# Kernel optimization log

Measured on AMD Instinct MI355X. Metric: run time of the kernel, lower is better.

Reference implementation:

```python
import jax, jax.numpy as jnp
import numpy as np

N = 768       # num nodes
E = 12288     # num edges (avg degree 16)
D_IN = 6
H = 256       # hidden_dim
TEMPERATURE = 1.0


def gcn_conv(x, W, b, src, dst, n):
    """PyG GCNConv: add self-loops, symmetric deg^-1/2 normalization, then xW aggregation + bias."""
    h = x @ W  # [n, H]
    loop = jnp.arange(n, dtype=src.dtype)
    s = jnp.concatenate([src, loop])
    d = jnp.concatenate([dst, loop])
    deg = jax.ops.segment_sum(jnp.ones(s.shape, dtype=h.dtype), d, num_segments=n)
    dinv = jnp.where(deg > 0, jax.lax.rsqrt(deg), 0.0)
    norm = dinv[s] * dinv[d]  # [E+n]
    out = jax.ops.segment_sum(h[s] * norm[:, None], d, num_segments=n)
    return out + b


def setup_inputs() -> dict:
    key = jax.random.key(0)
    ks = jax.random.split(key, 10)
    sc = lambda fan: np.float32(1.0 / np.sqrt(fan))
    x = jax.random.normal(ks[0], (N, D_IN), jnp.float32)
    edge_index = jax.random.randint(ks[1], (2, E), 0, N, dtype=jnp.int32)
    Wc1 = jax.random.normal(ks[2], (D_IN, H), jnp.float32) * sc(D_IN)
    bc1 = jnp.zeros((H,), jnp.float32)
    Wc2 = jax.random.normal(ks[3], (H, H), jnp.float32) * sc(H)
    bc2 = jnp.zeros((H,), jnp.float32)
    We1 = jax.random.normal(ks[4], (2 * H, H), jnp.float32) * sc(2 * H)
    be1 = jax.random.normal(ks[5], (H,), jnp.float32) * sc(2 * H)
    We2 = jax.random.normal(ks[6], (H, 1), jnp.float32) * sc(H)
    be2 = jax.random.normal(ks[7], (1,), jnp.float32) * sc(H)
    return {"x": x, "edge_index": edge_index, "Wc1": Wc1, "bc1": bc1,
            "Wc2": Wc2, "bc2": bc2, "We1": We1, "be1": be1, "We2": We2, "be2": be2}


def reference(x, edge_index, Wc1, bc1, Wc2, bc2, We1, be1, We2, be2):
    src, dst = edge_index[0], edge_index[1]
    h = jax.nn.elu(gcn_conv(x, Wc1, bc1, src, dst, N))
    h = gcn_conv(h, Wc2, bc2, src, dst, N)  # [N, H]
    # edge scorer: Linear(cat([x_i, x_j])) == x_i @ We1[:H] + x_j @ We1[H:] + be1
    ai = h @ We1[:H]   # [N, H], contribution of x_i (row node)
    aj = h @ We1[H:]   # [N, H], contribution of x_j (col node)
    pair = jax.nn.relu(ai[:, None, :] + aj[None, :, :] + be1)  # [N, N, H]
    logits = jnp.einsum('ijh,h->ij', pair, We2[:, 0]) + be2[0]  # [N, N]
    logits = logits / TEMPERATURE
    logits = jnp.where(jnp.eye(N, dtype=bool), -jnp.inf, logits)
    return jax.nn.softmax(logits, axis=-1)
```

## Files before the change

### kernel.cpp

```cpp
#include <hip/hip_runtime.h>
#include <math.h>

#define N_NODES 768
#define N_EDGES 12288
#define D_INF 6
#define H 256
#define CAP 128
#define LC 256

__global__ __launch_bounds__(256) void k_prep(
    const float* __restrict__ x, const int* __restrict__ ei,
    const float* __restrict__ Wc1, const float* __restrict__ bc1,
    int* __restrict__ cnt_g, int* __restrict__ slots, float* __restrict__ h1) {
    __shared__ int s_cnt[N_NODES];
    __shared__ int s_list[LC];
    __shared__ int s_nm, s_pos[3];
    __shared__ float s_agg[3][D_INF];
    const int t = threadIdx.x, b = blockIdx.x, v0 = b * 3;
    const int* src = ei;
    const int* dst = ei + N_EDGES;

    for (int v = t; v < N_NODES; v += 256) s_cnt[v] = 0;
    if (t == 0) s_nm = 0;
    if (t < 3) s_pos[t] = 0;
    if (t < 3 * D_INF) ((float*)s_agg)[t] = 0.f;
    __syncthreads();
    for (int e = t; e < N_EDGES; e += 256) {
        int d = dst[e];
        atomicAdd(&s_cnt[d], 1);
        unsigned li = (unsigned)(d - v0);
        if (li < 3u) {
            int p = atomicAdd(&s_nm, 1);
            if (p < LC) s_list[p] = (src[e] << 2) | (int)li;
        }
    }
    __syncthreads();
    const int nm = min(s_nm, LC);
    if (t < 3) cnt_g[v0 + t] = s_cnt[v0 + t];
    for (int m = t; m < nm; m += 256) {
        int pk = s_list[m];
        int s = pk >> 2, li = pk & 3;
        int p = atomicAdd(&s_pos[li], 1);
        if (p < CAP) slots[(v0 + li) * CAP + p] = s;
        float w = rsqrtf((float)(s_cnt[s] + 1)) * rsqrtf((float)(s_cnt[v0 + li] + 1));
        #pragma unroll
        for (int k = 0; k < D_INF; ++k)
            atomicAdd(&s_agg[li][k], w * x[s * D_INF + k]);
    }
    if (t < 3) {
        int v = v0 + t;
        float dv2 = 1.0f / (float)(s_cnt[v] + 1);
        #pragma unroll
        for (int k = 0; k < D_INF; ++k)
            atomicAdd(&s_agg[t][k], dv2 * x[v * D_INF + k]);
    }
    __syncthreads();
    #pragma unroll
    for (int r = 0; r < 3; ++r) {
        float acc = bc1[t];
        #pragma unroll
        for (int k = 0; k < D_INF; ++k)
            acc = fmaf(s_agg[r][k], Wc1[k * H + t], acc);
        h1[(v0 + r) * H + t] = (acc > 0.f) ? acc : expm1f(acc);
    }
}

__global__ __launch_bounds__(1024) void k_mid(
    const float* __restrict__ h1, const int* __restrict__ cnt,
    const int* __restrict__ slots, const float* __restrict__ Wc2,
    const float* __restrict__ bc2, const float* __restrict__ We1,
    const float* __restrict__ be1, float* __restrict__ aib,
    float* __restrict__ ajcT) {
    __shared__ int   s_s[3][CAP];
    __shared__ float s_w[3][CAP];
    __shared__ int   s_cc[3];
    __shared__ float s_dv[3];
    __shared__ __align__(16) float s_agg[3][H];
    __shared__ __align__(16) float s_h2[3][H];
    __shared__ __align__(16) float s_part[16][6][H];
    const int t = threadIdx.x, b = blockIdx.x;
    const int q = t >> 8, tc = t & 255;
    const int lane = t & 63, w = t >> 6;
    const int v0 = b * 3, k0 = w * 16;

    if (t < 3) {
        int c = cnt[v0 + t];
        s_cc[t] = min(c, CAP);
        s_dv[t] = rsqrtf((float)(c + 1));
    }
    __syncthreads();
    if (q < 3) {
        int ccq = s_cc[q];
        for (int i = tc; i < ccq; i += 256) {
            int s = slots[(v0 + q) * CAP + i];
            s_s[q][i] = s;
            s_w[q][i] = rsqrtf((float)(cnt[s] + 1)) * s_dv[q];
        }
    }
    __syncthreads();

    if (q < 3) {
        float dv = s_dv[q];
        float acc = dv * dv * h1[(size_t)(v0 + q) * H + tc];
        int ccq = s_cc[q];
        #pragma unroll 4
        for (int n = 0; n < ccq; ++n)
            acc = fmaf(s_w[q][n], h1[(size_t)s_s[q][n] * H + tc], acc);
        s_agg[q][tc] = acc;
    }
    __syncthreads();

    {
        float a[3][16];
        #pragma unroll
        for (int r = 0; r < 3; ++r)
            #pragma unroll
            for (int qq = 0; qq < 4; ++qq) {
                float4 v = *(const float4*)&s_agg[r][k0 + qq * 4];
                a[r][qq * 4 + 0] = v.x; a[r][qq * 4 + 1] = v.y;
                a[r][qq * 4 + 2] = v.z; a[r][qq * 4 + 3] = v.w;
            }
        float4 c0 = {0.f, 0.f, 0.f, 0.f}, c1 = c0, c2 = c0;
        #pragma unroll
        for (int kk = 0; kk < 16; ++kk) {
            float4 wv = *(const float4*)(Wc2 + (size_t)(k0 + kk) * H + (lane << 2));
            c0.x = fmaf(a[0][kk], wv.x, c0.x); c0.y = fmaf(a[0][kk], wv.y, c0.y);
            c0.z = fmaf(a[0][kk], wv.z, c0.z); c0.w = fmaf(a[0][kk], wv.w, c0.w);
            c1.x = fmaf(a[1][kk], wv.x, c1.x); c1.y = fmaf(a[1][kk], wv.y, c1.y);
            c1.z = fmaf(a[1][kk], wv.z, c1.z); c1.w = fmaf(a[1][kk], wv.w, c1.w);
            c2.x = fmaf(a[2][kk], wv.x, c2.x); c2.y = fmaf(a[2][kk], wv.y, c2.y);
            c2.z = fmaf(a[2][kk], wv.z, c2.z); c2.w = fmaf(a[2][kk], wv.w, c2.w);
        }
        *(float4*)&s_part[w][0][lane << 2] = c0;
        *(float4*)&s_part[w][1][lane << 2] = c1;
        *(float4*)&s_part[w][2][lane << 2] = c2;
    }
    __syncthreads();
    if (t < 3 * H) {
        int r = t >> 8, c = t & 255;
        float v = bc2[c];
        #pragma unroll
        for (int ww = 0; ww < 16; ++ww) v += s_part[ww][r][c];
        s_h2[r][c] = v;
    }
    __syncthreads();

    {
        float a[3][16];
        #pragma unroll
        for (int r = 0; r < 3; ++r)
            #pragma unroll
            for (int qq = 0; qq < 4; ++qq) {
                float4 v = *(const float4*)&s_h2[r][k0 + qq * 4];
                a[r][qq * 4 + 0] = v.x; a[r][qq * 4 + 1] = v.y;
                a[r][qq * 4 + 2] = v.z; a[r][qq * 4 + 3] = v.w;
            }
        float4 ca0 = {0.f, 0.f, 0.f, 0.f}, ca1 = ca0, ca2 = ca0;
        float4 cb0 = ca0, cb1 = ca0, cb2 = ca0;
        #pragma unroll
        for (int kk = 0; kk < 16; ++kk) {
            int k = k0 + kk;
            float4 wa = *(const float4*)(We1 + (size_t)k * H + (lane << 2));
            float4 wb = *(const float4*)(We1 + (size_t)(H + k) * H + (lane << 2));
            ca0.x = fmaf(a[0][kk], wa.x, ca0.x); ca0.y = fmaf(a[0][kk], wa.y, ca0.y);
            ca0.z = fmaf(a[0][kk], wa.z, ca0.z); ca0.w = fmaf(a[0][kk], wa.w, ca0.w);
            ca1.x = fmaf(a[1][kk], wa.x, ca1.x); ca1.y = fmaf(a[1][kk], wa.y, ca1.y);
            ca1.z = fmaf(a[1][kk], wa.z, ca1.z); ca1.w = fmaf(a[1][kk], wa.w, ca1.w);
            ca2.x = fmaf(a[2][kk], wa.x, ca2.x); ca2.y = fmaf(a[2][kk], wa.y, ca2.y);
            ca2.z = fmaf(a[2][kk], wa.z, ca2.z); ca2.w = fmaf(a[2][kk], wa.w, ca2.w);
            cb0.x = fmaf(a[0][kk], wb.x, cb0.x); cb0.y = fmaf(a[0][kk], wb.y, cb0.y);
            cb0.z = fmaf(a[0][kk], wb.z, cb0.z); cb0.w = fmaf(a[0][kk], wb.w, cb0.w);
            cb1.x = fmaf(a[1][kk], wb.x, cb1.x); cb1.y = fmaf(a[1][kk], wb.y, cb1.y);
            cb1.z = fmaf(a[1][kk], wb.z, cb1.z); cb1.w = fmaf(a[1][kk], wb.w, cb1.w);
            cb2.x = fmaf(a[2][kk], wb.x, cb2.x); cb2.y = fmaf(a[2][kk], wb.y, cb2.y);
            cb2.z = fmaf(a[2][kk], wb.z, cb2.z); cb2.w = fmaf(a[2][kk], wb.w, cb2.w);
        }
        *(float4*)&s_part[w][0][lane << 2] = ca0;
        *(float4*)&s_part[w][1][lane << 2] = ca1;
        *(float4*)&s_part[w][2][lane << 2] = ca2;
        *(float4*)&s_part[w][3][lane << 2] = cb0;
        *(float4*)&s_part[w][4][lane << 2] = cb1;
        *(float4*)&s_part[w][5][lane << 2] = cb2;
    }
    __syncthreads();
    for (int idx = t; idx < 6 * H; idx += 1024) {
        int r6 = idx >> 8, c = idx & 255;
        float v = 0.f;
        #pragma unroll
        for (int ww = 0; ww < 16; ++ww) v += s_part[ww][r6][c];
        if (r6 < 3) aib[(size_t)(v0 + r6) * H + c] = v;
        else        ajcT[(size_t)c * N_NODES + v0 + (r6 - 3)] = v + be1[c];
    }
}

__global__ __launch_bounds__(512) void k_pair2(
    const float* __restrict__ aib, const float* __restrict__ ajcT,
    const float* __restrict__ We2, float* __restrict__ out) {
    __shared__ float s_ai[3 * H];
    __shared__ float s_w2[H];
    __shared__ __align__(16) float s_p[8 * 3 * N_NODES];
    __shared__ float s_lg[3 * N_NODES];
    __shared__ float red[3 * 256];
    const int t = threadIdx.x, b = blockIdx.x;
    const int lane = t & 63, w = t >> 6;
    const int i0 = b * 3, h0 = w * 32;

    for (int i = t; i < 3 * H; i += 512)
        s_ai[i] = aib[(size_t)(i0 + (i >> 8)) * H + (i & 255)];
    if (t < H) s_w2[t] = We2[t];
    __syncthreads();

    float4 acc[3][3];
    #pragma unroll
    for (int r = 0; r < 3; ++r)
        #pragma unroll
        for (int jj = 0; jj < 3; ++jj)
            acc[r][jj] = make_float4(0.f, 0.f, 0.f, 0.f);

    #pragma unroll 4
    for (int hh = 0; hh < 32; ++hh) {
        int h = h0 + hh;
        float wv = s_w2[h];
        float a0 = s_ai[h], a1 = s_ai[H + h], a2 = s_ai[2 * H + h];
        const float* col = ajcT + (size_t)h * N_NODES + (lane << 2);
        #pragma unroll
        for (int jj = 0; jj < 3; ++jj) {
            float4 bv = *(const float4*)(col + jj * 256);
            acc[0][jj].x = fmaf(fmaxf(a0 + bv.x, 0.f), wv, acc[0][jj].x);
            acc[0][jj].y = fmaf(fmaxf(a0 + bv.y, 0.f), wv, acc[0][jj].y);
            acc[0][jj].z = fmaf(fmaxf(a0 + bv.z, 0.f), wv, acc[0][jj].z);
            acc[0][jj].w = fmaf(fmaxf(a0 + bv.w, 0.f), wv, acc[0][jj].w);
            acc[1][jj].x = fmaf(fmaxf(a1 + bv.x, 0.f), wv, acc[1][jj].x);
            acc[1][jj].y = fmaf(fmaxf(a1 + bv.y, 0.f), wv, acc[1][jj].y);
            acc[1][jj].z = fmaf(fmaxf(a1 + bv.z, 0.f), wv, acc[1][jj].z);
            acc[1][jj].w = fmaf(fmaxf(a1 + bv.w, 0.f), wv, acc[1][jj].w);
            acc[2][jj].x = fmaf(fmaxf(a2 + bv.x, 0.f), wv, acc[2][jj].x);
            acc[2][jj].y = fmaf(fmaxf(a2 + bv.y, 0.f), wv, acc[2][jj].y);
            acc[2][jj].z = fmaf(fmaxf(a2 + bv.z, 0.f), wv, acc[2][jj].z);
            acc[2][jj].w = fmaf(fmaxf(a2 + bv.w, 0.f), wv, acc[2][jj].w);
        }
    }
    #pragma unroll
    for (int r = 0; r < 3; ++r)
        #pragma unroll
        for (int jj = 0; jj < 3; ++jj)
            *(float4*)&s_p[(w * 3 + r) * N_NODES + jj * 256 + (lane << 2)] = acc[r][jj];
    __syncthreads();

    for (int idx = t; idx < 3 * N_NODES; idx += 512) {
        int r = idx / N_NODES, j = idx - r * N_NODES;
        float v = 0.f;
        #pragma unroll
        for (int ww = 0; ww < 8; ++ww) v += s_p[(ww * 3 + r) * N_NODES + j];
        s_lg[idx] = (j == i0 + r) ? -INFINITY : v;
    }
    __syncthreads();

    const int tc = t & 255, th = t >> 8;
    if (th == 0) {
        red[tc] = fmaxf(fmaxf(s_lg[tc], s_lg[tc + 256]), s_lg[tc + 512]);
        red[512 + tc] = fmaxf(fmaxf(s_lg[1536 + tc], s_lg[1536 + tc + 256]),
                              s_lg[1536 + tc + 512]);
    } else {
        red[256 + tc] = fmaxf(fmaxf(s_lg[768 + tc], s_lg[768 + tc + 256]),
                              s_lg[768 + tc + 512]);
    }
    __syncthreads();
    for (int s = 128; s > 0; s >>= 1) {
        if (th == 0 && tc < s) {
            red[tc] = fmaxf(red[tc], red[tc + s]);
            red[512 + tc] = fmaxf(red[512 + tc], red[512 + tc + s]);
        } else if (th == 1 && tc < s) {
            red[256 + tc] = fmaxf(red[256 + tc], red[256 + tc + s]);
        }
        __syncthreads();
    }
    float mx0 = red[0], mx1 = red[256], mx2 = red[512];
    __syncthreads();
    if (th == 0) {
        red[tc] = __expf(s_lg[tc] - mx0) + __expf(s_lg[tc + 256] - mx0)
                + __expf(s_lg[tc + 512] - mx0);
        red[512 + tc] = __expf(s_lg[1536 + tc] - mx2) + __expf(s_lg[1536 + tc + 256] - mx2)
                      + __expf(s_lg[1536 + tc + 512] - mx2);
    } else {
        red[256 + tc] = __expf(s_lg[768 + tc] - mx1) + __expf(s_lg[768 + tc + 256] - mx1)
                      + __expf(s_lg[768 + tc + 512] - mx1);
    }
    __syncthreads();
    for (int s = 128; s > 0; s >>= 1) {
        if (th == 0 && tc < s) {
            red[tc] += red[tc + s];
            red[512 + tc] += red[512 + tc + s];
        } else if (th == 1 && tc < s) {
            red[256 + tc] += red[256 + tc + s];
        }
        __syncthreads();
    }
    float iv0 = 1.0f / red[0], iv1 = 1.0f / red[256], iv2 = 1.0f / red[512];

    for (int idx = t; idx < 3 * N_NODES; idx += 512) {
        int r = idx / N_NODES, j = idx - r * N_NODES;
        float m = (r == 0) ? mx0 : (r == 1) ? mx1 : mx2;
        float iv = (r == 0) ? iv0 : (r == 1) ? iv1 : iv2;
        out[(size_t)(i0 + r) * N_NODES + j] = __expf(s_lg[idx] - m) * iv;
    }
}

extern "C" void kernel_launch(void* const* d_in, const int* in_sizes, int n_in,
                              void* d_out, int out_size, void* d_ws, size_t ws_size,
                              hipStream_t stream) {
    const float* x   = (const float*)d_in[0];
    const int*   ei  = (const int*)d_in[1];
    const float* Wc1 = (const float*)d_in[2];
    const float* bc1 = (const float*)d_in[3];
    const float* Wc2 = (const float*)d_in[4];
    const float* bc2 = (const float*)d_in[5];
    const float* We1 = (const float*)d_in[6];
    const float* be1 = (const float*)d_in[7];
    const float* We2 = (const float*)d_in[8];
    float* out = (float*)d_out;

    char* ws = (char*)d_ws;
    int*   cnt  = (int*)(ws + 0);
    int*   slots= (int*)(ws + 4096);
    float* h1   = (float*)(ws + 397312);
    float* aib  = (float*)(ws + 1183744);
    float* ajcT = (float*)(ws + 1970176);

    k_prep<<<N_NODES / 3, 256, 0, stream>>>(x, ei, Wc1, bc1, cnt, slots, h1);
    k_mid<<<N_NODES / 3, 1024, 0, stream>>>(h1, cnt, slots, Wc2, bc2, We1, be1,
                                            aib, ajcT);
    k_pair2<<<N_NODES / 3, 512, 0, stream>>>(aib, ajcT, We2, out);
}
```

Measured before the change: 52.47 us.

## Fold Wc2 into We1 to skip the intermediate h2 matmul

Computes a combined weight Wc2·[We1a|We1b] and a combined bias in 64 extra blocks of the prep kernel, so the mid kernel needs one 3x256x512 matmul instead of two dependent matmuls with a reduction and sync between them. The fold is recomputed on every call from the weights, so no work is carried across calls. The warps' k and h slice starts are also rotated by block index, probably to spread simultaneous weight reads across addresses. The cost is the serial 256-step weight fold inside the prep launch, which may lengthen that kernel's critical path.

Result: slower. 67.99 us (+29.6%).

```diff
diff --git a/kernel.cpp b/kernel.cpp
--- a/kernel.cpp
+++ b/kernel.cpp
@@ -11,77 +11,118 @@
 __global__ __launch_bounds__(256) void k_prep(
     const float* __restrict__ x, const int* __restrict__ ei,
     const float* __restrict__ Wc1, const float* __restrict__ bc1,
-    int* __restrict__ cnt_g, int* __restrict__ slots, float* __restrict__ h1) {
-    __shared__ int s_cnt[N_NODES];
-    __shared__ int s_list[LC];
-    __shared__ int s_nm, s_pos[3];
-    __shared__ float s_agg[3][D_INF];
-    const int t = threadIdx.x, b = blockIdx.x, v0 = b * 3;
-    const int* src = ei;
-    const int* dst = ei + N_EDGES;
-
-    for (int v = t; v < N_NODES; v += 256) s_cnt[v] = 0;
-    if (t == 0) s_nm = 0;
-    if (t < 3) s_pos[t] = 0;
-    if (t < 3 * D_INF) ((float*)s_agg)[t] = 0.f;
-    __syncthreads();
-    for (int e = t; e < N_EDGES; e += 256) {
-        int d = dst[e];
-        atomicAdd(&s_cnt[d], 1);
-        unsigned li = (unsigned)(d - v0);
-        if (li < 3u) {
-            int p = atomicAdd(&s_nm, 1);
-            if (p < LC) s_list[p] = (src[e] << 2) | (int)li;
-        }
-    }
-    __syncthreads();
-    const int nm = min(s_nm, LC);
-    if (t < 3) cnt_g[v0 + t] = s_cnt[v0 + t];
-    for (int m = t; m < nm; m += 256) {
-        int pk = s_list[m];
-        int s = pk >> 2, li = pk & 3;
-        int p = atomicAdd(&s_pos[li], 1);
-        if (p < CAP) slots[(v0 + li) * CAP + p] = s;
-        float w = rsqrtf((float)(s_cnt[s] + 1)) * rsqrtf((float)(s_cnt[v0 + li] + 1));
-        #pragma unroll
-        for (int k = 0; k < D_INF; ++k)
-            atomicAdd(&s_agg[li][k], w * x[s * D_INF + k]);
-    }
-    if (t < 3) {
-        int v = v0 + t;
-        float dv2 = 1.0f / (float)(s_cnt[v] + 1);
-        #pragma unroll
-        for (int k = 0; k < D_INF; ++k)
-            atomicAdd(&s_agg[t][k], dv2 * x[v * D_INF + k]);
-    }
-    __syncthreads();
-    #pragma unroll
-    for (int r = 0; r < 3; ++r) {
-        float acc = bc1[t];
-        #pragma unroll
-        for (int k = 0; k < D_INF; ++k)
-            acc = fmaf(s_agg[r][k], Wc1[k * H + t], acc);
-        h1[(v0 + r) * H + t] = (acc > 0.f) ? acc : expm1f(acc);
+    const float* __restrict__ Wc2, const float* __restrict__ bc2,
+    const float* __restrict__ We1, const float* __restrict__ be1,
+    int* __restrict__ cnt_g, int* __restrict__ slots, float* __restrict__ h1,
+    float* __restrict__ Wcombo, float* __restrict__ bias_c) {
+    const int t = threadIdx.x;
+    if (blockIdx.x < 256) {
+        __shared__ int s_cnt[N_NODES];
+        __shared__ int s_list[LC];
+        __shared__ int s_nm, s_pos[3];
+        __shared__ float s_agg[3][D_INF];
+        const int b = blockIdx.x, v0 = b * 3;
+        const int* src = ei;
+        const int* dst = ei + N_EDGES;
+
+        for (int v = t; v < N_NODES; v += 256) s_cnt[v] = 0;
+        if (t == 0) s_nm = 0;
+        if (t < 3) s_pos[t] = 0;
+        if (t < 3 * D_INF) ((float*)s_agg)[t] = 0.f;
+        __syncthreads();
+        for (int e = t; e < N_EDGES; e += 256) {
+            int d = dst[e];
+            atomicAdd(&s_cnt[d], 1);
+            unsigned li = (unsigned)(d - v0);
+            if (li < 3u) {
+                int p = atomicAdd(&s_nm, 1);
+                if (p < LC) s_list[p] = (src[e] << 2) | (int)li;
+            }
+        }
+        __syncthreads();
+        const int nm = min(s_nm, LC);
+        if (t < 3) cnt_g[v0 + t] = s_cnt[v0 + t];
+        for (int m = t; m < nm; m += 256) {
+            int pk = s_list[m];
+            int s = pk >> 2, li = pk & 3;
+            int p = atomicAdd(&s_pos[li], 1);
+            if (p < CAP) slots[(v0 + li) * CAP + p] = s;
+            float w = rsqrtf((float)(s_cnt[s] + 1)) * rsqrtf((float)(s_cnt[v0 + li] + 1));
+            #pragma unroll
+            for (int k = 0; k < D_INF; ++k)
+                atomicAdd(&s_agg[li][k], w * x[s * D_INF + k]);
+        }
+        if (t < 3) {
+            int v = v0 + t;
+            float dv2 = 1.0f / (float)(s_cnt[v] + 1);
+            #pragma unroll
+            for (int k = 0; k < D_INF; ++k)
+                atomicAdd(&s_agg[t][k], dv2 * x[v * D_INF + k]);
+        }
+        __syncthreads();
+        #pragma unroll
+        for (int r = 0; r < 3; ++r) {
+            float acc = bc1[t];
+            #pragma unroll
+            for (int k = 0; k < D_INF; ++k)
+                acc = fmaf(s_agg[r][k], Wc1[k * H + t], acc);
+            h1[(v0 + r) * H + t] = (acc > 0.f) ? acc : expm1f(acc);
+        }
+    } else {
+        const int ib = blockIdx.x - 256;
+        const int kt = ib >> 3, ot = ib & 7;
+        const int k0c = kt * 32, o0 = ot * 64;
+        const int oc4 = (t & 15) * 4, rg2 = t >> 4;
+        const float* wbase = (o0 < H) ? (We1 + o0 + oc4)
+                                      : (We1 + (size_t)H * H + (o0 - H) + oc4);
+        const int r0 = k0c + rg2 * 2;
+        float4 a0 = {0.f, 0.f, 0.f, 0.f}, a1 = a0;
+        for (int c = 0; c < H; ++c) {
+            float4 wv = *(const float4*)(wbase + (size_t)c * H);
+            float w0 = Wc2[(size_t)c * 0 + (size_t)(r0 + 0) * H + c];
+            float w1 = Wc2[(size_t)(r0 + 1) * H + c];
+            a0.x = fmaf(w0, wv.x, a0.x); a0.y = fmaf(w0, wv.y, a0.y);
+            a0.z = fmaf(w0, wv.z, a0.z); a0.w = fmaf(w0, wv.w, a0.w);
+            a1.x = fmaf(w1, wv.x, a1.x); a1.y = fmaf(w1, wv.y, a1.y);
+            a1.z = fmaf(w1, wv.z, a1.z); a1.w = fmaf(w1, wv.w, a1.w);
+        }
+        *(float4*)(Wcombo + (size_t)(r0 + 0) * 512 + o0 + oc4) = a0;
+        *(float4*)(Wcombo + (size_t)(r0 + 1) * 512 + o0 + oc4) = a1;
+        if (kt == 0 && t < 16) {
+            const float* wb2 = (o0 < H) ? (We1 + o0 + t * 4)
+                                        : (We1 + (size_t)H * H + (o0 - H) + t * 4);
+            float4 bs;
+            if (o0 >= H) {
+                bs.x = be1[o0 - H + t * 4 + 0]; bs.y = be1[o0 - H + t * 4 + 1];
+                bs.z = be1[o0 - H + t * 4 + 2]; bs.w = be1[o0 - H + t * 4 + 3];
+            } else bs = make_float4(0.f, 0.f, 0.f, 0.f);
+            for (int c = 0; c < H; ++c) {
+                float4 wv = *(const float4*)(wb2 + (size_t)c * H);
+                float bv = bc2[c];
+                bs.x = fmaf(bv, wv.x, bs.x); bs.y = fmaf(bv, wv.y, bs.y);
+                bs.z = fmaf(bv, wv.z, bs.z); bs.w = fmaf(bv, wv.w, bs.w);
+            }
+            *(float4*)(bias_c + o0 + t * 4) = bs;
+        }
     }
 }
 
 __global__ __launch_bounds__(1024) void k_mid(
     const float* __restrict__ h1, const int* __restrict__ cnt,
-    const int* __restrict__ slots, const float* __restrict__ Wc2,
-    const float* __restrict__ bc2, const float* __restrict__ We1,
-    const float* __restrict__ be1, float* __restrict__ aib,
+    const int* __restrict__ slots, const float* __restrict__ Wcombo,
+    const float* __restrict__ bias_c, float* __restrict__ aib,
     float* __restrict__ ajcT) {
     __shared__ int   s_s[3][CAP];
     __shared__ float s_w[3][CAP];
     __shared__ int   s_cc[3];
     __shared__ float s_dv[3];
     __shared__ __align__(16) float s_agg[3][H];
-    __shared__ __align__(16) float s_h2[3][H];
     __shared__ __align__(16) float s_part[16][6][H];
     const int t = threadIdx.x, b = blockIdx.x;
     const int q = t >> 8, tc = t & 255;
     const int lane = t & 63, w = t >> 6;
-    const int v0 = b * 3, k0 = w * 16;
+    const int v0 = b * 3;
+    const int k0 = ((w + b) & 15) * 16;
 
     if (t < 3) {
         int c = cnt[v0 + t];
@@ -120,48 +161,13 @@
                 a[r][qq * 4 + 0] = v.x; a[r][qq * 4 + 1] = v.y;
                 a[r][qq * 4 + 2] = v.z; a[r][qq * 4 + 3] = v.w;
             }
-        float4 c0 = {0.f, 0.f, 0.f, 0.f}, c1 = c0, c2 = c0;
-        #pragma unroll
-        for (int kk = 0; kk < 16; ++kk) {
-            float4 wv = *(const float4*)(Wc2 + (size_t)(k0 + kk) * H + (lane << 2));
-            c0.x = fmaf(a[0][kk], wv.x, c0.x); c0.y = fmaf(a[0][kk], wv.y, c0.y);
-            c0.z = fmaf(a[0][kk], wv.z, c0.z); c0.w = fmaf(a[0][kk], wv.w, c0.w);
-            c1.x = fmaf(a[1][kk], wv.x, c1.x); c1.y = fmaf(a[1][kk], wv.y, c1.y);
-            c1.z = fmaf(a[1][kk], wv.z, c1.z); c1.w = fmaf(a[1][kk], wv.w, c1.w);
-            c2.x = fmaf(a[2][kk], wv.x, c2.x); c2.y = fmaf(a[2][kk], wv.y, c2.y);
-            c2.z = fmaf(a[2][kk], wv.z, c2.z); c2.w = fmaf(a[2][kk], wv.w, c2.w);
-        }
-        *(float4*)&s_part[w][0][lane << 2] = c0;
-        *(float4*)&s_part[w][1][lane << 2] = c1;
-        *(float4*)&s_part[w][2][lane << 2] = c2;
-    }
-    __syncthreads();
-    if (t < 3 * H) {
-        int r = t >> 8, c = t & 255;
-        float v = bc2[c];
-        #pragma unroll
-        for (int ww = 0; ww < 16; ++ww) v += s_part[ww][r][c];
-        s_h2[r][c] = v;
-    }
-    __syncthreads();
-
-    {
-        float a[3][16];
-        #pragma unroll
-        for (int r = 0; r < 3; ++r)
-            #pragma unroll
-            for (int qq = 0; qq < 4; ++qq) {
-                float4 v = *(const float4*)&s_h2[r][k0 + qq * 4];
-                a[r][qq * 4 + 0] = v.x; a[r][qq * 4 + 1] = v.y;
-                a[r][qq * 4 + 2] = v.z; a[r][qq * 4 + 3] = v.w;
-            }
         float4 ca0 = {0.f, 0.f, 0.f, 0.f}, ca1 = ca0, ca2 = ca0;
         float4 cb0 = ca0, cb1 = ca0, cb2 = ca0;
         #pragma unroll
         for (int kk = 0; kk < 16; ++kk) {
             int k = k0 + kk;
-            float4 wa = *(const float4*)(We1 + (size_t)k * H + (lane << 2));
-            float4 wb = *(const float4*)(We1 + (size_t)(H + k) * H + (lane << 2));
+            float4 wa = *(const float4*)(Wcombo + (size_t)k * 512 + (lane << 2));
+            float4 wb = *(const float4*)(Wcombo + (size_t)k * 512 + 256 + (lane << 2));
             ca0.x = fmaf(a[0][kk], wa.x, ca0.x); ca0.y = fmaf(a[0][kk], wa.y, ca0.y);
             ca0.z = fmaf(a[0][kk], wa.z, ca0.z); ca0.w = fmaf(a[0][kk], wa.w, ca0.w);
             ca1.x = fmaf(a[1][kk], wa.x, ca1.x); ca1.y = fmaf(a[1][kk], wa.y, ca1.y);
@@ -188,8 +194,8 @@
         float v = 0.f;
         #pragma unroll
         for (int ww = 0; ww < 16; ++ww) v += s_part[ww][r6][c];
-        if (r6 < 3) aib[(size_t)(v0 + r6) * H + c] = v;
-        else        ajcT[(size_t)c * N_NODES + v0 + (r6 - 3)] = v + be1[c];
+        if (r6 < 3) aib[(size_t)(v0 + r6) * H + c] = v + bias_c[c];
+        else        ajcT[(size_t)c * N_NODES + v0 + (r6 - 3)] = v + bias_c[H + c];
     }
 }
 
@@ -203,7 +209,8 @@
     __shared__ float red[3 * 256];
     const int t = threadIdx.x, b = blockIdx.x;
     const int lane = t & 63, w = t >> 6;
-    const int i0 = b * 3, h0 = w * 32;
+    const int i0 = b * 3;
+    const int h0 = ((w + b) & 7) * 32;
 
     for (int i = t; i < 3 * H; i += 512)
         s_ai[i] = aib[(size_t)(i0 + (i >> 8)) * H + (i & 255)];
@@ -321,14 +328,17 @@
     float* out = (float*)d_out;
 
     char* ws = (char*)d_ws;
-    int*   cnt  = (int*)(ws + 0);
-    int*   slots= (int*)(ws + 4096);
-    float* h1   = (float*)(ws + 397312);
-    float* aib  = (float*)(ws + 1183744);
-    float* ajcT = (float*)(ws + 1970176);
-
-    k_prep<<<N_NODES / 3, 256, 0, stream>>>(x, ei, Wc1, bc1, cnt, slots, h1);
-    k_mid<<<N_NODES / 3, 1024, 0, stream>>>(h1, cnt, slots, Wc2, bc2, We1, be1,
+    int*   cnt    = (int*)(ws + 0);
+    int*   slots  = (int*)(ws + 4096);
+    float* h1     = (float*)(ws + 397312);
+    float* aib    = (float*)(ws + 1183744);
+    float* ajcT   = (float*)(ws + 1970176);
+    float* Wcombo = (float*)(ws + 2756608);
+    float* bias_c = (float*)(ws + 3280896);
+
+    k_prep<<<320, 256, 0, stream>>>(x, ei, Wc1, bc1, Wc2, bc2, We1, be1,
+                                    cnt, slots, h1, Wcombo, bias_c);
+    k_mid<<<N_NODES / 3, 1024, 0, stream>>>(h1, cnt, slots, Wcombo, bias_c,
                                             aib, ajcT);
     k_pair2<<<N_NODES / 3, 512, 0, stream>>>(aib, ajcT, We2, out);
 }
```

## Recompute first-layer hidden features on the fly from 6-wide aggregates

Applied to the files above, without the earlier changes.

k_prep now writes only the 6-dim aggregated input per node instead of the 256-wide ELU(GW+b) hidden layer. k_mid stages all aggregates plus Wc1 and bc1 in shared memory and recomputes h1 for each neighbor inside the gather loop. This removes the 768x256 h1 write and the scattered global reads of h1 rows. In exchange each neighbor costs 6 FMAs and an expm1, and shared memory use in k_mid grows by about 26KB, which may lower occupancy.

Result: slower. 54.12 us (+3.1%).

```diff
diff --git a/kernel.cpp b/kernel.cpp
--- a/kernel.cpp
+++ b/kernel.cpp
@@ -10,8 +10,7 @@
 
 __global__ __launch_bounds__(256) void k_prep(
     const float* __restrict__ x, const int* __restrict__ ei,
-    const float* __restrict__ Wc1, const float* __restrict__ bc1,
-    int* __restrict__ cnt_g, int* __restrict__ slots, float* __restrict__ h1) {
+    int* __restrict__ cnt_g, int* __restrict__ slots, float* __restrict__ G) {
     __shared__ int s_cnt[N_NODES];
     __shared__ int s_list[LC];
     __shared__ int s_nm, s_pos[3];
@@ -55,19 +54,13 @@
             atomicAdd(&s_agg[t][k], dv2 * x[v * D_INF + k]);
     }
     __syncthreads();
-    #pragma unroll
-    for (int r = 0; r < 3; ++r) {
-        float acc = bc1[t];
-        #pragma unroll
-        for (int k = 0; k < D_INF; ++k)
-            acc = fmaf(s_agg[r][k], Wc1[k * H + t], acc);
-        h1[(v0 + r) * H + t] = (acc > 0.f) ? acc : expm1f(acc);
-    }
+    if (t < 3 * D_INF) G[v0 * D_INF + t] = ((float*)s_agg)[t];
 }
 
 __global__ __launch_bounds__(1024) void k_mid(
-    const float* __restrict__ h1, const int* __restrict__ cnt,
-    const int* __restrict__ slots, const float* __restrict__ Wc2,
+    const float* __restrict__ G, const int* __restrict__ cnt,
+    const int* __restrict__ slots, const float* __restrict__ Wc1,
+    const float* __restrict__ bc1, const float* __restrict__ Wc2,
     const float* __restrict__ bc2, const float* __restrict__ We1,
     const float* __restrict__ be1, float* __restrict__ aib,
     float* __restrict__ ajcT) {
@@ -75,6 +68,9 @@
     __shared__ float s_w[3][CAP];
     __shared__ int   s_cc[3];
     __shared__ float s_dv[3];
+    __shared__ float s_G[N_NODES * D_INF];
+    __shared__ float s_Wc1[D_INF * H];
+    __shared__ float s_bc1[H];
     __shared__ __align__(16) float s_agg[3][H];
     __shared__ __align__(16) float s_h2[3][H];
     __shared__ __align__(16) float s_part[16][6][H];
@@ -83,6 +79,9 @@
     const int lane = t & 63, w = t >> 6;
     const int v0 = b * 3, k0 = w * 16;
 
+    for (int i = t; i < N_NODES * D_INF; i += 1024) s_G[i] = G[i];
+    for (int i = t; i < D_INF * H; i += 1024) s_Wc1[i] = Wc1[i];
+    if (t < H) s_bc1[t] = bc1[t];
     if (t < 3) {
         int c = cnt[v0 + t];
         s_cc[t] = min(c, CAP);
@@ -101,11 +100,22 @@
 
     if (q < 3) {
         float dv = s_dv[q];
-        float acc = dv * dv * h1[(size_t)(v0 + q) * H + tc];
+        float a0 = s_bc1[tc];
+        #pragma unroll
+        for (int k = 0; k < D_INF; ++k)
+            a0 = fmaf(s_G[(v0 + q) * D_INF + k], s_Wc1[k * H + tc], a0);
+        float hv = (a0 > 0.f) ? a0 : expm1f(a0);
+        float acc = dv * dv * hv;
         int ccq = s_cc[q];
-        #pragma unroll 4
-        for (int n = 0; n < ccq; ++n)
-            acc = fmaf(s_w[q][n], h1[(size_t)s_s[q][n] * H + tc], acc);
+        for (int n = 0; n < ccq; ++n) {
+            int s = s_s[q][n];
+            float a = s_bc1[tc];
+            #pragma unroll
+            for (int k = 0; k < D_INF; ++k)
+                a = fmaf(s_G[s * D_INF + k], s_Wc1[k * H + tc], a);
+            float h = (a > 0.f) ? a : expm1f(a);
+            acc = fmaf(s_w[q][n], h, acc);
+        }
         s_agg[q][tc] = acc;
     }
     __syncthreads();
@@ -321,14 +331,14 @@
     float* out = (float*)d_out;
 
     char* ws = (char*)d_ws;
-    int*   cnt  = (int*)(ws + 0);
-    int*   slots= (int*)(ws + 4096);
-    float* h1   = (float*)(ws + 397312);
-    float* aib  = (float*)(ws + 1183744);
-    float* ajcT = (float*)(ws + 1970176);
-
-    k_prep<<<N_NODES / 3, 256, 0, stream>>>(x, ei, Wc1, bc1, cnt, slots, h1);
-    k_mid<<<N_NODES / 3, 1024, 0, stream>>>(h1, cnt, slots, Wc2, bc2, We1, be1,
-                                            aib, ajcT);
+    int*   cnt   = (int*)(ws + 0);
+    int*   slots = (int*)(ws + 4096);
+    float* G     = (float*)(ws + 397312);
+    float* aib   = (float*)(ws + 417792);
+    float* ajcT  = (float*)(ws + 1204224);
+
+    k_prep<<<N_NODES / 3, 256, 0, stream>>>(x, ei, cnt, slots, G);
+    k_mid<<<N_NODES / 3, 1024, 0, stream>>>(G, cnt, slots, Wc1, bc1, Wc2, bc2,
+                                            We1, be1, aib, ajcT);
     k_pair2<<<N_NODES / 3, 512, 0, stream>>>(aib, ajcT, We2, out);
 }
```
